# Optimization experiments

Hardware: AMD Instinct MI355X
Metric: run time of the kernel (lower is better)

The kernel has to match this reference:

```python
import jax, jax.numpy as jnp
import numpy as np

NF4 = jnp.array([-1.0, -0.6961928009986877, -0.5250730514526367, -0.39491748809814453,
                 -0.28444138169288635, -0.18477343022823334, -0.09105003625154495, 0.0,
                 0.07958029955625534, 0.16093020141124725, 0.24611230194568634,
                 0.33791524171829224, 0.44070982933044434, 0.5626170039176941,
                 0.7229568362236023, 1.0], dtype=jnp.float32)
BLOCK_SIZE = 64
SCALING = 32.0 / 16.0  # alpha / rank


def setup_inputs() -> dict:
    key = jax.random.key(0)
    k = jax.random.split(key, 6)
    B, S, IN, OUT, R = 4, 128, 4096, 11008, 16
    n_blocks = (OUT * IN) // BLOCK_SIZE  # 704512, exact (no padding needed)
    return {
        "x": jax.random.normal(k[0], (B, S, IN), jnp.float32),
        "weight_indices": jax.random.randint(k[1], (OUT, IN), 0, 16, dtype=jnp.int32),
        "weight_scales": jax.random.uniform(k[2], (n_blocks,), jnp.float32),
        "lora_A": jax.random.normal(k[3], (IN, R), jnp.float32),
        "lora_B": jax.random.normal(k[4], (R, OUT), jnp.float32),
        "bias": jax.random.normal(k[5], (OUT,), jnp.float32),
    }


def dequantize_nf4(indices, scales, shape):
    # LUT gather then blockwise absmax scale
    w = NF4[indices.reshape(-1)]                    # [out*in]
    w = w.reshape(-1, BLOCK_SIZE) * scales[:, None]  # [n_blocks, block]
    return w.reshape(shape)                          # [out, in]


def reference(x, weight_indices, weight_scales, lora_A, lora_B, bias):
    W = dequantize_nf4(weight_indices, weight_scales, weight_indices.shape)  # [out, in]
    base = jnp.einsum("bsi,oi->bso", x, W) + bias                            # F.linear
    lora = (x @ lora_A) @ lora_B                                             # low-rank path (dropout p=0 -> identity)
    return base + lora * SCALING
```

## Files before the change

### kernel.cpp

```cpp
#include <hip/hip_runtime.h>
#include <stdint.h>

typedef __bf16 bf16x8 __attribute__((ext_vector_type(8)));
typedef float f32x4 __attribute__((ext_vector_type(4)));
typedef unsigned short ushort_t;

#define N_OUT 11008
#define K_DIM 4096
#define M_DIM 512
#define BM 256
#define BN 64
#define BK 32
#define NK_TILES 128
#define LDB 40

__constant__ float c_nf4[16] = {
    -1.0f, -0.6961928009986877f, -0.5250730514526367f, -0.39491748809814453f,
    -0.28444138169288635f, -0.18477343022823334f, -0.09105003625154495f, 0.0f,
    0.07958029955625534f, 0.16093020141124725f, 0.24611230194568634f,
    0.33791524171829224f, 0.44070982933044434f, 0.5626170039176941f,
    0.7229568362236023f, 1.0f};

__device__ __forceinline__ uint32_t pkbf(float lo, float hi) {
  uint32_t ul = __builtin_bit_cast(uint32_t, lo);
  uint32_t uh = __builtin_bit_cast(uint32_t, hi);
  return ((ul + 0x8000u) >> 16) | ((uh + 0x8000u) & 0xffff0000u);
}

__device__ __forceinline__ void async16(const void* g, void* l) {
  __builtin_amdgcn_global_load_lds(
      (const __attribute__((address_space(1))) void*)g,
      (__attribute__((address_space(3))) void*)l, 16, 0, 0);
}

__device__ __forceinline__ bf16x8 ldfrag(const ushort_t* p) {
  uint4 r = *reinterpret_cast<const uint4*>(p);
  return __builtin_bit_cast(bf16x8, r);
}

__global__ void k_cvt_x(const float* __restrict__ x, ushort_t* __restrict__ xbf) {
  int i = blockIdx.x * blockDim.x + threadIdx.x;
  const float4* xp = reinterpret_cast<const float4*>(x) + (size_t)i * 2;
  float4 v0 = xp[0], v1 = xp[1];
  uint4 o;
  o.x = pkbf(v0.x, v0.y);
  o.y = pkbf(v0.z, v0.w);
  o.z = pkbf(v1.x, v1.y);
  o.w = pkbf(v1.z, v1.w);
  reinterpret_cast<uint4*>(xbf)[i] = o;
}

__global__ void k_xa(const float* __restrict__ x, const float* __restrict__ lA,
                     ushort_t* __restrict__ xap) {
  int m = blockIdx.x;
  int t = threadIdx.x;
  int r = t & 15, part = t >> 4;
  const float* xr = x + (size_t)m * K_DIM + part * 256;
  const float* ar = lA + (size_t)(part * 256) * 16 + r;
  float acc = 0.f;
#pragma unroll 8
  for (int k = 0; k < 256; ++k) acc += xr[k] * ar[(size_t)k * 16];
  __shared__ float red[16][17];
  red[part][r] = acc;
  __syncthreads();
  if (t < 32) {
    float v = 0.f;
    if (t < 16) {
      for (int p = 0; p < 16; ++p) v += red[p][t];
      v *= 2.0f;
    }
    uint32_t u = __builtin_bit_cast(uint32_t, v);
    xap[(size_t)m * 32 + t] = (ushort_t)((u + 0x8000u) >> 16);
  }
}

__global__ void k_bt(const float* __restrict__ lB, ushort_t* __restrict__ btp) {
  int o = blockIdx.x * blockDim.x + threadIdx.x;
  uint32_t p[8];
#pragma unroll
  for (int j = 0; j < 8; ++j)
    p[j] = pkbf(lB[(size_t)(2 * j) * N_OUT + o], lB[(size_t)(2 * j + 1) * N_OUT + o]);
  uint4* dst = reinterpret_cast<uint4*>(btp + (size_t)o * 32);
  dst[0] = make_uint4(p[0], p[1], p[2], p[3]);
  dst[1] = make_uint4(p[4], p[5], p[6], p[7]);
  dst[2] = make_uint4(0u, 0u, 0u, 0u);
  dst[3] = make_uint4(0u, 0u, 0u, 0u);
}

__launch_bounds__(256, 2)
__global__ void k_main(const ushort_t* __restrict__ xbf, const int* __restrict__ wi,
                       const float* __restrict__ sc, const ushort_t* __restrict__ xap,
                       const ushort_t* __restrict__ btp, const float* __restrict__ bias,
                       float* __restrict__ out) {
  __shared__ __align__(16) ushort_t lds_a[BM * BK];
  __shared__ __align__(16) ushort_t lds_b[BN * LDB];
  __shared__ float lutf[16];

  const int t = threadIdx.x;
  const int lane = t & 63;
  const int w = t >> 6;
  const int o0 = blockIdx.x * BN;
  const int m0 = blockIdx.y * BM;

  if (t < 16) lutf[t] = c_nf4[t];

  const int kb = (lane & 3) * 8;
  const ushort_t* ga[4];
#pragma unroll
  for (int j = 0; j < 4; ++j) {
    int arow = (j * 4 + w) * 16 + (lane >> 2);
    ga[j] = xbf + (size_t)(m0 + arow) * K_DIM + kb;
  }

  const int ro = t >> 2;
  const int q4 = (t & 3) * 8;
  const int* gb = wi + (size_t)(o0 + ro) * K_DIM + q4;
  const float* gs = sc + (size_t)(o0 + ro) * 64;
  ushort_t* lb_dst = lds_b + ro * LDB + q4;

  const ushort_t* af_base = lds_a + (w * 64 + (lane & 15)) * BK + (lane >> 4) * 8;
  const ushort_t* bf_base = lds_b + (lane & 15) * LDB + (lane >> 4) * 8;

  f32x4 acc[4][4];
#pragma unroll
  for (int mi = 0; mi < 4; ++mi)
#pragma unroll
    for (int ni = 0; ni < 4; ++ni) acc[mi][ni] = (f32x4){0.f, 0.f, 0.f, 0.f};

  int4 i0 = ((const int4*)gb)[0];
  int4 i1 = ((const int4*)gb)[1];
  float s = gs[0];
  gb += BK;

  for (int kt = 0; kt < NK_TILES + 1; ++kt) {
    __syncthreads();
    if (kt < NK_TILES) {
#pragma unroll
      for (int j = 0; j < 4; ++j) {
        async16(ga[j], lds_a + (j * 4 + w) * 512 + lane * 8);
        ga[j] += BK;
      }
      uint32_t p0 = pkbf(lutf[i0.x] * s, lutf[i0.y] * s);
      uint32_t p1 = pkbf(lutf[i0.z] * s, lutf[i0.w] * s);
      uint32_t p2 = pkbf(lutf[i1.x] * s, lutf[i1.y] * s);
      uint32_t p3 = pkbf(lutf[i1.z] * s, lutf[i1.w] * s);
      *reinterpret_cast<uint4*>(lb_dst) = make_uint4(p0, p1, p2, p3);
      if (kt + 1 < NK_TILES) {
        i0 = ((const int4*)gb)[0];
        i1 = ((const int4*)gb)[1];
        s = gs[(kt + 1) >> 1];
        gb += BK;
      }
    } else {
#pragma unroll
      for (int j = 0; j < 4; ++j) {
        int arow = (j * 4 + w) * 16 + (lane >> 2);
        async16(xap + (size_t)(m0 + arow) * 32 + kb,
                lds_a + (j * 4 + w) * 512 + lane * 8);
      }
      uint4 bv = *reinterpret_cast<const uint4*>(btp + (size_t)(o0 + ro) * 32 + q4);
      *reinterpret_cast<uint4*>(lb_dst) = bv;
    }
    __syncthreads();

    bf16x8 av[4], bv[4];
#pragma unroll
    for (int mi = 0; mi < 4; ++mi) av[mi] = ldfrag(af_base + mi * 16 * BK);
#pragma unroll
    for (int ni = 0; ni < 4; ++ni) bv[ni] = ldfrag(bf_base + ni * 16 * LDB);
#pragma unroll
    for (int mi = 0; mi < 4; ++mi)
#pragma unroll
      for (int ni = 0; ni < 4; ++ni)
        acc[mi][ni] =
            __builtin_amdgcn_mfma_f32_16x16x32_bf16(av[mi], bv[ni], acc[mi][ni], 0, 0, 0);
  }

  const int cl = lane & 15, rg = (lane >> 4) * 4;
#pragma unroll
  for (int ni = 0; ni < 4; ++ni) {
    int col = o0 + ni * 16 + cl;
    float bvs = bias[col];
#pragma unroll
    for (int mi = 0; mi < 4; ++mi) {
      int row0 = m0 + w * 64 + mi * 16 + rg;
      float* op = out + (size_t)row0 * N_OUT + col;
#pragma unroll
      for (int i = 0; i < 4; ++i) op[(size_t)i * N_OUT] = acc[mi][ni][i] + bvs;
    }
  }
}

extern "C" void kernel_launch(void* const* d_in, const int* in_sizes, int n_in,
                              void* d_out, int out_size, void* d_ws, size_t ws_size,
                              hipStream_t stream) {
  const float* x = (const float*)d_in[0];
  const int* wi = (const int*)d_in[1];
  const float* sc = (const float*)d_in[2];
  const float* lA = (const float*)d_in[3];
  const float* lB = (const float*)d_in[4];
  const float* bias = (const float*)d_in[5];
  float* out = (float*)d_out;

  char* wsb = (char*)d_ws;
  ushort_t* xbf = (ushort_t*)wsb;
  ushort_t* xap = (ushort_t*)(wsb + (4u << 20));
  ushort_t* btp = (ushort_t*)(wsb + (4u << 20) + (32u << 10));

  k_cvt_x<<<1024, 256, 0, stream>>>(x, xbf);
  k_xa<<<M_DIM, 256, 0, stream>>>(x, lA, xap);
  k_bt<<<43, 256, 0, stream>>>(lB, btp);
  dim3 grid(N_OUT / BN, M_DIM / BM);
  k_main<<<grid, 256, 0, stream>>>(xbf, wi, sc, xap, btp, bias, out);
}
```

Measured before the change: 397.4 us.

## Split-K main GEMM with atomics, fuse prep kernels, widen BK, swizzle A tiles

Merges the three prep kernels into one launch that also writes bias into the output, then runs the main GEMM split over K in two halves with atomicAdd accumulation. BK doubles to 64, the x tile is XOR-swizzled so LDS reads avoid bank conflicts, and a paired 256-entry LUT dequantizes two NF4 values per lookup. The aim is to double the grid for better CU occupancy, with fewer launches and fewer syncs per K. In exchange it pays for atomic float adds to the output and an extra pass writing bias, and results are no longer bitwise deterministic.

Result: faster. 357.4 us (-10.1%).

```diff
diff --git a/kernel.cpp b/kernel.cpp
--- a/kernel.cpp
+++ b/kernel.cpp
@@ -10,9 +10,9 @@
 #define M_DIM 512
 #define BM 256
 #define BN 64
-#define BK 32
-#define NK_TILES 128
-#define LDB 40
+#define BK 64
+#define KHALF 2048
+#define NT 32
 
 __constant__ float c_nf4[16] = {
     -1.0f, -0.6961928009986877f, -0.5250730514526367f, -0.39491748809814453f,
@@ -38,88 +38,117 @@
   return __builtin_bit_cast(bf16x8, r);
 }
 
-__global__ void k_cvt_x(const float* __restrict__ x, ushort_t* __restrict__ xbf) {
-  int i = blockIdx.x * blockDim.x + threadIdx.x;
-  const float4* xp = reinterpret_cast<const float4*>(x) + (size_t)i * 2;
-  float4 v0 = xp[0], v1 = xp[1];
-  uint4 o;
-  o.x = pkbf(v0.x, v0.y);
-  o.y = pkbf(v0.z, v0.w);
-  o.z = pkbf(v1.x, v1.y);
-  o.w = pkbf(v1.z, v1.w);
-  reinterpret_cast<uint4*>(xbf)[i] = o;
-}
-
-__global__ void k_xa(const float* __restrict__ x, const float* __restrict__ lA,
-                     ushort_t* __restrict__ xap) {
-  int m = blockIdx.x;
-  int t = threadIdx.x;
-  int r = t & 15, part = t >> 4;
-  const float* xr = x + (size_t)m * K_DIM + part * 256;
-  const float* ar = lA + (size_t)(part * 256) * 16 + r;
-  float acc = 0.f;
-#pragma unroll 8
-  for (int k = 0; k < 256; ++k) acc += xr[k] * ar[(size_t)k * 16];
-  __shared__ float red[16][17];
-  red[part][r] = acc;
-  __syncthreads();
-  if (t < 32) {
-    float v = 0.f;
-    if (t < 16) {
-      for (int p = 0; p < 16; ++p) v += red[p][t];
-      v *= 2.0f;
-    }
-    uint32_t u = __builtin_bit_cast(uint32_t, v);
-    xap[(size_t)m * 32 + t] = (ushort_t)((u + 0x8000u) >> 16);
-  }
-}
-
-__global__ void k_bt(const float* __restrict__ lB, ushort_t* __restrict__ btp) {
-  int o = blockIdx.x * blockDim.x + threadIdx.x;
-  uint32_t p[8];
-#pragma unroll
-  for (int j = 0; j < 8; ++j)
-    p[j] = pkbf(lB[(size_t)(2 * j) * N_OUT + o], lB[(size_t)(2 * j + 1) * N_OUT + o]);
-  uint4* dst = reinterpret_cast<uint4*>(btp + (size_t)o * 32);
-  dst[0] = make_uint4(p[0], p[1], p[2], p[3]);
-  dst[1] = make_uint4(p[4], p[5], p[6], p[7]);
-  dst[2] = make_uint4(0u, 0u, 0u, 0u);
-  dst[3] = make_uint4(0u, 0u, 0u, 0u);
-}
-
-__launch_bounds__(256, 2)
+__device__ __forceinline__ uint32_t dq2(int a, int b, float s, const float2* lut) {
+  float2 l = lut[a | (b << 4)];
+  return pkbf(l.x * s, l.y * s);
+}
+
+__global__ void k_prep(const float* __restrict__ x, const float* __restrict__ lA,
+                       const float* __restrict__ lB, const float* __restrict__ bias,
+                       ushort_t* __restrict__ xbf, ushort_t* __restrict__ xap,
+                       ushort_t* __restrict__ btp, float* __restrict__ out) {
+  const int b = blockIdx.x, t = threadIdx.x;
+  if (b < 1024) {
+    int oc = b * 256 + t;
+    int m = oc >> 9;
+    int cr = oc & 511;
+    int win = cr >> 3, cp = cr & 7;
+    int c = cp ^ (m & 7);
+    const float4* s4 = (const float4*)(x + (size_t)m * K_DIM + win * 64 + c * 8);
+    float4 v0 = s4[0], v1 = s4[1];
+    uint4 o;
+    o.x = pkbf(v0.x, v0.y);
+    o.y = pkbf(v0.z, v0.w);
+    o.z = pkbf(v1.x, v1.y);
+    o.w = pkbf(v1.z, v1.w);
+    ((uint4*)xbf)[oc] = o;
+  } else if (b < 1536) {
+    __shared__ float red[256 * 17];
+    int m = b - 1024;
+    int ks = t * 16;
+    alignas(16) float xs[16];
+    const f32x4* xv = (const f32x4*)(x + (size_t)m * K_DIM + ks);
+    ((f32x4*)xs)[0] = xv[0];
+    ((f32x4*)xs)[1] = xv[1];
+    ((f32x4*)xs)[2] = xv[2];
+    ((f32x4*)xs)[3] = xv[3];
+    f32x4 ac0 = 0.f, ac1 = 0.f, ac2 = 0.f, ac3 = 0.f;
+#pragma unroll
+    for (int kk = 0; kk < 16; ++kk) {
+      float xk = xs[kk];
+      const f32x4* l4 = (const f32x4*)(lA + (size_t)(ks + kk) * 16);
+      ac0 += xk * l4[0];
+      ac1 += xk * l4[1];
+      ac2 += xk * l4[2];
+      ac3 += xk * l4[3];
+    }
+#pragma unroll
+    for (int r = 0; r < 4; ++r) {
+      red[t * 17 + r] = ac0[r];
+      red[t * 17 + 4 + r] = ac1[r];
+      red[t * 17 + 8 + r] = ac2[r];
+      red[t * 17 + 12 + r] = ac3[r];
+    }
+    __syncthreads();
+#pragma unroll
+    for (int s = 128; s >= 16; s >>= 1) {
+      if (t < s)
+        for (int r = 0; r < 16; ++r) red[t * 17 + r] += red[(t + s) * 17 + r];
+      __syncthreads();
+    }
+    if (t < 32) {
+      float v = 0.f;
+      if (t < 16) {
+        for (int p = 0; p < 16; ++p) v += red[p * 17 + t];
+        v *= 2.0f;
+      }
+      uint32_t u = __builtin_bit_cast(uint32_t, v);
+      xap[(size_t)m * 32 + t] = (ushort_t)((u + 0x8000u) >> 16);
+    }
+  } else if (b < 1579) {
+    int o = (b - 1536) * 256 + t;
+    uint32_t p[8];
+#pragma unroll
+    for (int j = 0; j < 8; ++j)
+      p[j] = pkbf(lB[(size_t)(2 * j) * N_OUT + o], lB[(size_t)(2 * j + 1) * N_OUT + o]);
+    uint4* dst = reinterpret_cast<uint4*>(btp + (size_t)o * 32);
+    dst[0] = make_uint4(p[0], p[1], p[2], p[3]);
+    dst[1] = make_uint4(p[4], p[5], p[6], p[7]);
+    dst[2] = make_uint4(0u, 0u, 0u, 0u);
+    dst[3] = make_uint4(0u, 0u, 0u, 0u);
+  } else {
+    int i = (b - 1579) * 256 + t;
+    int col4 = i % 2752;
+    ((float4*)out)[i] = ((const float4*)bias)[col4];
+  }
+}
+
+__launch_bounds__(256, 3)
 __global__ void k_main(const ushort_t* __restrict__ xbf, const int* __restrict__ wi,
                        const float* __restrict__ sc, const ushort_t* __restrict__ xap,
-                       const ushort_t* __restrict__ btp, const float* __restrict__ bias,
-                       float* __restrict__ out) {
+                       const ushort_t* __restrict__ btp, float* __restrict__ out) {
   __shared__ __align__(16) ushort_t lds_a[BM * BK];
-  __shared__ __align__(16) ushort_t lds_b[BN * LDB];
-  __shared__ float lutf[16];
+  __shared__ __align__(16) ushort_t lds_b[BN * 72];
+  __shared__ float2 lutp[256];
 
   const int t = threadIdx.x;
   const int lane = t & 63;
   const int w = t >> 6;
   const int o0 = blockIdx.x * BN;
   const int m0 = blockIdx.y * BM;
-
-  if (t < 16) lutf[t] = c_nf4[t];
-
-  const int kb = (lane & 3) * 8;
-  const ushort_t* ga[4];
-#pragma unroll
-  for (int j = 0; j < 4; ++j) {
-    int arow = (j * 4 + w) * 16 + (lane >> 2);
-    ga[j] = xbf + (size_t)(m0 + arow) * K_DIM + kb;
-  }
-
-  const int ro = t >> 2;
-  const int q4 = (t & 3) * 8;
-  const int* gb = wi + (size_t)(o0 + ro) * K_DIM + q4;
-  const float* gs = sc + (size_t)(o0 + ro) * 64;
-  ushort_t* lb_dst = lds_b + ro * LDB + q4;
-
-  const ushort_t* af_base = lds_a + (w * 64 + (lane & 15)) * BK + (lane >> 4) * 8;
-  const ushort_t* bf_base = lds_b + (lane & 15) * LDB + (lane >> 4) * 8;
+  const int kh = blockIdx.z;
+  const int k0 = kh * KHALF;
+
+  lutp[t] = make_float2(c_nf4[t & 15], c_nf4[t >> 4]);
+
+  const int brow = t >> 2, bq = t & 3;
+  const int* gb = wi + (size_t)(o0 + brow) * K_DIM + k0 + bq * 16;
+  const float* gs = sc + (size_t)(o0 + brow) * 64 + kh * 32;
+  ushort_t* lb = lds_b + brow * 72 + bq * 16;
+
+  const ushort_t* ga =
+      xbf + (size_t)(m0 + w * 64 + (lane >> 3)) * K_DIM + k0 + (lane & 7) * 8;
+  ushort_t* la_dst = lds_a + w * 4096 + lane * 8;
 
   f32x4 acc[4][4];
 #pragma unroll
@@ -127,66 +156,94 @@
 #pragma unroll
     for (int ni = 0; ni < 4; ++ni) acc[mi][ni] = (f32x4){0.f, 0.f, 0.f, 0.f};
 
-  int4 i0 = ((const int4*)gb)[0];
-  int4 i1 = ((const int4*)gb)[1];
+  int4 bi0 = ((const int4*)gb)[0], bi1 = ((const int4*)gb)[1];
+  int4 bi2 = ((const int4*)gb)[2], bi3 = ((const int4*)gb)[3];
   float s = gs[0];
   gb += BK;
-
-  for (int kt = 0; kt < NK_TILES + 1; ++kt) {
-    __syncthreads();
-    if (kt < NK_TILES) {
-#pragma unroll
-      for (int j = 0; j < 4; ++j) {
-        async16(ga[j], lds_a + (j * 4 + w) * 512 + lane * 8);
-        ga[j] += BK;
-      }
-      uint32_t p0 = pkbf(lutf[i0.x] * s, lutf[i0.y] * s);
-      uint32_t p1 = pkbf(lutf[i0.z] * s, lutf[i0.w] * s);
-      uint32_t p2 = pkbf(lutf[i1.x] * s, lutf[i1.y] * s);
-      uint32_t p3 = pkbf(lutf[i1.z] * s, lutf[i1.w] * s);
-      *reinterpret_cast<uint4*>(lb_dst) = make_uint4(p0, p1, p2, p3);
-      if (kt + 1 < NK_TILES) {
-        i0 = ((const int4*)gb)[0];
-        i1 = ((const int4*)gb)[1];
-        s = gs[(kt + 1) >> 1];
-        gb += BK;
-      }
-    } else {
-#pragma unroll
-      for (int j = 0; j < 4; ++j) {
-        int arow = (j * 4 + w) * 16 + (lane >> 2);
-        async16(xap + (size_t)(m0 + arow) * 32 + kb,
-                lds_a + (j * 4 + w) * 512 + lane * 8);
-      }
-      uint4 bv = *reinterpret_cast<const uint4*>(btp + (size_t)(o0 + ro) * 32 + q4);
-      *reinterpret_cast<uint4*>(lb_dst) = bv;
-    }
-    __syncthreads();
-
+  uint4 braw;
+
+  const ushort_t* afb = lds_a + (w * 64 + (lane & 15)) * BK;
+  const int q = lane >> 4;
+  const ushort_t* bfb = lds_b + (lane & 15) * 72 + q * 8;
+
+#pragma unroll 1
+  for (int kt = 0; kt < NT; ++kt) {
+    __syncthreads();
+    uint4 w0, w1;
+    w0.x = dq2(bi0.x, bi0.y, s, lutp);
+    w0.y = dq2(bi0.z, bi0.w, s, lutp);
+    w0.z = dq2(bi1.x, bi1.y, s, lutp);
+    w0.w = dq2(bi1.z, bi1.w, s, lutp);
+    w1.x = dq2(bi2.x, bi2.y, s, lutp);
+    w1.y = dq2(bi2.z, bi2.w, s, lutp);
+    w1.z = dq2(bi3.x, bi3.y, s, lutp);
+    w1.w = dq2(bi3.z, bi3.w, s, lutp);
+    *reinterpret_cast<uint4*>(lb) = w0;
+    *reinterpret_cast<uint4*>(lb + 8) = w1;
+#pragma unroll
+    for (int j = 0; j < 8; ++j)
+      async16(ga + (size_t)j * 8 * K_DIM + kt * BK, la_dst + j * 512);
+    __syncthreads();
+    if (kt + 1 < NT) {
+      bi0 = ((const int4*)gb)[0];
+      bi1 = ((const int4*)gb)[1];
+      bi2 = ((const int4*)gb)[2];
+      bi3 = ((const int4*)gb)[3];
+      s = gs[kt + 1];
+      gb += BK;
+    } else if (kh == 1) {
+      braw = *reinterpret_cast<const uint4*>(btp + (size_t)(o0 + brow) * 32 + bq * 8);
+    }
+#pragma unroll
+    for (int kc = 0; kc < 2; ++kc) {
+      const int cpr = ((kc * 4 + q) ^ (lane & 7)) * 8;
+      bf16x8 av[4], bv[4];
+#pragma unroll
+      for (int mi = 0; mi < 4; ++mi) av[mi] = ldfrag(afb + mi * 16 * BK + cpr);
+#pragma unroll
+      for (int ni = 0; ni < 4; ++ni) bv[ni] = ldfrag(bfb + ni * 16 * 72 + kc * 32);
+#pragma unroll
+      for (int mi = 0; mi < 4; ++mi)
+#pragma unroll
+        for (int ni = 0; ni < 4; ++ni)
+          acc[mi][ni] = __builtin_amdgcn_mfma_f32_16x16x32_bf16(av[mi], bv[ni],
+                                                                acc[mi][ni], 0, 0, 0);
+    }
+  }
+
+  if (kh == 1) {
+    __syncthreads();
+    *reinterpret_cast<uint4*>(lds_b + brow * 72 + bq * 8) = braw;
+#pragma unroll
+    for (int j = 0; j < 4; ++j)
+      async16(xap + (size_t)(m0 + w * 64 + j * 16 + (lane >> 2)) * 32 + (lane & 3) * 8,
+              lds_a + w * 2048 + j * 512 + lane * 8);
+    __syncthreads();
     bf16x8 av[4], bv[4];
 #pragma unroll
-    for (int mi = 0; mi < 4; ++mi) av[mi] = ldfrag(af_base + mi * 16 * BK);
-#pragma unroll
-    for (int ni = 0; ni < 4; ++ni) bv[ni] = ldfrag(bf_base + ni * 16 * LDB);
-#pragma unroll
     for (int mi = 0; mi < 4; ++mi)
+      av[mi] = ldfrag(lds_a + w * 2048 + (mi * 16 + (lane & 15)) * 32 + q * 8);
+#pragma unroll
+    for (int ni = 0; ni < 4; ++ni)
+      bv[ni] = ldfrag(lds_b + (ni * 16 + (lane & 15)) * 72 + q * 8);
+#pragma unroll
+    for (int mi = 0; mi < 4; ++mi)
 #pragma unroll
       for (int ni = 0; ni < 4; ++ni)
-        acc[mi][ni] =
-            __builtin_amdgcn_mfma_f32_16x16x32_bf16(av[mi], bv[ni], acc[mi][ni], 0, 0, 0);
-  }
-
-  const int cl = lane & 15, rg = (lane >> 4) * 4;
+        acc[mi][ni] = __builtin_amdgcn_mfma_f32_16x16x32_bf16(av[mi], bv[ni],
+                                                              acc[mi][ni], 0, 0, 0);
+  }
+
+  const int cl = lane & 15, rg = q * 4;
 #pragma unroll
   for (int ni = 0; ni < 4; ++ni) {
     int col = o0 + ni * 16 + cl;
-    float bvs = bias[col];
 #pragma unroll
     for (int mi = 0; mi < 4; ++mi) {
       int row0 = m0 + w * 64 + mi * 16 + rg;
       float* op = out + (size_t)row0 * N_OUT + col;
 #pragma unroll
-      for (int i = 0; i < 4; ++i) op[(size_t)i * N_OUT] = acc[mi][ni][i] + bvs;
+      for (int i = 0; i < 4; ++i) atomicAdd(op + (size_t)i * N_OUT, acc[mi][ni][i]);
     }
   }
 }
@@ -207,9 +264,7 @@
   ushort_t* xap = (ushort_t*)(wsb + (4u << 20));
   ushort_t* btp = (ushort_t*)(wsb + (4u << 20) + (32u << 10));
 
-  k_cvt_x<<<1024, 256, 0, stream>>>(x, xbf);
-  k_xa<<<M_DIM, 256, 0, stream>>>(x, lA, xap);
-  k_bt<<<43, 256, 0, stream>>>(lB, btp);
-  dim3 grid(N_OUT / BN, M_DIM / BM);
-  k_main<<<grid, 256, 0, stream>>>(xbf, wi, sc, xap, btp, bias, out);
-}
+  k_prep<<<7083, 256, 0, stream>>>(x, lA, lB, bias, xbf, xap, btp, out);
+  dim3 grid(N_OUT / BN, M_DIM / BM, 2);
+  k_main<<<grid, 256, 0, stream>>>(xbf, wi, sc, xap, btp, out);
+}
```
